# Performance work log

Measured on AMD Instinct MI355X. Metric: run time of the kernel, lower is better.

Reference implementation:

```python
import jax, jax.numpy as jnp
import numpy as np

N = 100_000        # nodes
E = 1_600_000      # edges (avg degree 16)
IN_DIM = 256
OUT_DIM = 32
HEADS = 4
EDGE_DIM = 64
NUM_ETYPES = 8
NEG_SLOPE = 0.2


def setup_inputs() -> dict:
    key = jax.random.key(0)
    ks = jax.random.split(key, 12)
    h = jax.random.normal(ks[0], (N, IN_DIM), dtype=jnp.float32)
    row = jax.random.randint(ks[1], (E,), 0, N, dtype=jnp.int32)
    col = jax.random.randint(ks[2], (E,), 0, N, dtype=jnp.int32)
    etype = jax.random.randint(ks[3], (E,), 0, NUM_ETYPES, dtype=jnp.int32)
    # learned parameters (xavier-ish scale)
    W = jax.random.normal(ks[4], (IN_DIM, OUT_DIM * HEADS), dtype=jnp.float32) * 0.08
    edge_emb = jax.random.normal(ks[5], (NUM_ETYPES, EDGE_DIM), dtype=jnp.float32) * 0.2
    Wr = jax.random.normal(ks[6], (NUM_ETYPES, EDGE_DIM, EDGE_DIM * HEADS), dtype=jnp.float32) * 0.1
    a_l = jax.random.normal(ks[7], (1, HEADS, OUT_DIM), dtype=jnp.float32) * 0.3
    a_r = jax.random.normal(ks[8], (1, HEADS, OUT_DIM), dtype=jnp.float32) * 0.3
    a_e = jax.random.normal(ks[9], (1, HEADS, EDGE_DIM), dtype=jnp.float32) * 0.3
    res_W = jax.random.normal(ks[10], (IN_DIM, OUT_DIM * HEADS), dtype=jnp.float32) * 0.08
    res_b = jnp.zeros((OUT_DIM * HEADS,), dtype=jnp.float32)
    return dict(h=h, W=W, edge_emb=edge_emb, Wr=Wr, a_l=a_l, a_r=a_r, a_e=a_e,
                res_W=res_W, res_b=res_b, row=row, col=col, etype=etype)


def reference(h, W, edge_emb, Wr, a_l, a_r, a_e, res_W, res_b, row, col, etype):
    n = h.shape[0]
    heads, out_dim = a_l.shape[1], a_l.shape[2]
    edge_dim = a_e.shape[2]
    n_etypes = edge_emb.shape[0]

    # node transform: [N, H, D]
    emb = (h @ W).reshape(n, heads, out_dim)
    emb = jnp.where(jnp.isnan(emb), 0.0, emb)

    # typed linear on edge-type embeddings; only num_etypes distinct rows,
    # so compute per type then gather per edge (same math as W_r(edge_emb[etype]))
    e_trans = jnp.einsum('te,tef->tf', edge_emb, Wr).reshape(n_etypes, heads, edge_dim)
    h_e_type = (a_e * e_trans).sum(-1)            # [T, H]

    h_l = (a_l * emb).sum(-1)                     # [N, H]
    h_r = (a_r * emb).sum(-1)                     # [N, H]

    att = h_l[row] + h_r[col] + h_e_type[etype]   # [E, H]
    att = jnp.where(att > 0, att, NEG_SLOPE * att)  # leaky relu

    # edge softmax grouped by destination node (col)
    seg_max = jax.ops.segment_max(att, col, num_segments=n)   # [N, H]
    ex = jnp.exp(att - seg_max[col])
    seg_sum = jax.ops.segment_sum(ex, col, num_segments=n)    # [N, H]
    alpha = ex / seg_sum[col]                                  # [E, H]

    # u_mul_e + sum aggregation; emb permuted to [N, D, H] as in the original
    emb_p = emb.transpose(0, 2, 1)                 # [N, D, H]
    msg = emb_p[row] * alpha[:, None, :]           # [E, D, H]
    agg = jax.ops.segment_sum(msg, col, num_segments=n)  # [N, D, H]
    h_out = agg.reshape(n, out_dim * heads)

    h_out = h_out + h @ res_W + res_b              # residual linear
    return jax.nn.elu(h_out)
```

## Files before the change

kernel.cpp:

```cpp
#include <hip/hip_runtime.h>
#include <math.h>

#define N_NODES   100000
#define N_EDGES   1600000
#define IN_DIM    256
#define OUT_DIM   32
#define HEADS     4
#define C_DIM     128
#define EDGE_DIM  64
#define NUM_ETY   8
#define NEG_SLOPE 0.2f
#define NBLK_SCAN 391
#define M_TILE    128
#define BSTRIDE   40

typedef __attribute__((ext_vector_type(8))) short s8b;
typedef __attribute__((ext_vector_type(4))) float f32x4;
typedef unsigned short ushort_t;

__device__ __forceinline__ short bf16rne(float x) {
    unsigned int u = __float_as_uint(x);
    unsigned int r = (u + 0x7FFFu + ((u >> 16) & 1u)) >> 16;
    return (short)r;
}

__global__ void kz_init(unsigned int* __restrict__ counts) {
    int i = blockIdx.x * blockDim.x + threadIdx.x;
    if (i < N_NODES) counts[i] = 0u;
}

__global__ __launch_bounds__(256) void k_het(
    const float* __restrict__ edge_emb, const float* __restrict__ Wr,
    const float* __restrict__ a_e, float* __restrict__ h_et) {
    __shared__ float ee[EDGE_DIM];
    const int t = threadIdx.x;
    const int ty = blockIdx.x;
    if (t < EDGE_DIM) ee[t] = edge_emb[ty * EDGE_DIM + t];
    __syncthreads();
    const int hh = t >> 6, f = t & 63;
    float acc = 0.f;
#pragma unroll 8
    for (int e = 0; e < EDGE_DIM; ++e)
        acc += ee[e] * Wr[(size_t)(ty * EDGE_DIM + e) * (HEADS * EDGE_DIM) + hh * EDGE_DIM + f];
    acc *= a_e[hh * EDGE_DIM + f];
#pragma unroll
    for (int m = 32; m >= 1; m >>= 1) acc += __shfl_xor(acc, m);
    if (f == 0) h_et[ty * HEADS + hh] = acc;
}

__global__ void kw_prep(const float* __restrict__ W, const float* __restrict__ resW,
                        short* __restrict__ wt) {
    int idx = blockIdx.x * 256 + threadIdx.x;
    int k = idx >> 8, c = idx & 255;
    float v = (c < C_DIM) ? W[k * C_DIM + c] : resW[k * C_DIM + (c - C_DIM)];
    wt[c * IN_DIM + k] = bf16rne(v);
}

__global__ __launch_bounds__(512, 2) void k1_mfma(
    const float* __restrict__ h, const short* __restrict__ wt,
    const float* __restrict__ resb,
    const float* __restrict__ a_l, const float* __restrict__ a_r,
    ushort_t* __restrict__ embh, float* __restrict__ hl, float* __restrict__ hr,
    float* __restrict__ out) {
    __shared__ short hs[M_TILE * IN_DIM];
    __shared__ short bs[2][256 * BSTRIDE];
    const int t  = threadIdx.x;
    const int n0 = blockIdx.x * M_TILE;

#pragma unroll
    for (int i = 0; i < 16; ++i) {
        int f4 = i * 512 + t;
        int row = f4 >> 6, q = f4 & 63;
        int rg = n0 + row;
        float4 v = make_float4(0.f, 0.f, 0.f, 0.f);
        if (rg < N_NODES) v = *(const float4*)&h[(size_t)rg * IN_DIM + q * 4];
        short4 b4;
        b4.x = bf16rne(v.x); b4.y = bf16rne(v.y);
        b4.z = bf16rne(v.z); b4.w = bf16rne(v.w);
        int idx = (row * IN_DIM + q * 4) ^ ((row & 7) << 3);
        *(short4*)&hs[idx] = b4;
    }

    {
        int c = t >> 1, hf = t & 1;
        const s8b* src = (const s8b*)&wt[c * IN_DIM + hf * 16];
        s8b v0 = src[0], v1 = src[1];
        *(s8b*)&bs[0][c * BSTRIDE + hf * 16] = v0;
        *(s8b*)&bs[0][c * BSTRIDE + hf * 16 + 8] = v1;
    }
    __syncthreads();

    const int lane = t & 63, w = t >> 6;
    const int wm = w >> 1;
    const int wn = w & 1;
    const int ln = lane & 15;
    const int kk = lane >> 4;
    const int cstage = t >> 1, hstage = t & 1;

    f32x4 acc[2][8];
#pragma unroll
    for (int mf = 0; mf < 2; ++mf)
#pragma unroll
        for (int nf = 0; nf < 8; ++nf) acc[mf][nf] = (f32x4){0.f, 0.f, 0.f, 0.f};

    int cur = 0;
#pragma unroll
    for (int ks = 0; ks < 8; ++ks) {
        s8b nb0 = {}, nb1 = {};
        if (ks < 7) {
            const s8b* src = (const s8b*)&wt[cstage * IN_DIM + (ks + 1) * 32 + hstage * 16];
            nb0 = src[0];
            nb1 = src[1];
        }

        int r0 = wm * 32 + ln;
        int r1 = wm * 32 + 16 + ln;
        int a0i = (r0 * IN_DIM + ks * 32 + kk * 8) ^ ((r0 & 7) << 3);
        int a1i = (r1 * IN_DIM + ks * 32 + kk * 8) ^ ((r1 & 7) << 3);
        s8b a0 = *(const s8b*)&hs[a0i];
        s8b a1 = *(const s8b*)&hs[a1i];

#pragma unroll
        for (int nf = 0; nf < 8; ++nf) {
            int c = wn * 128 + nf * 16 + ln;
            s8b b = *(const s8b*)&bs[cur][c * BSTRIDE + kk * 8];
            acc[0][nf] = __builtin_amdgcn_mfma_f32_16x16x32_bf16(a0, b, acc[0][nf], 0, 0, 0);
            acc[1][nf] = __builtin_amdgcn_mfma_f32_16x16x32_bf16(a1, b, acc[1][nf], 0, 0, 0);
        }

        if (ks < 7) {
            *(s8b*)&bs[cur ^ 1][cstage * BSTRIDE + hstage * 16] = nb0;
            *(s8b*)&bs[cur ^ 1][cstage * BSTRIDE + hstage * 16 + 8] = nb1;
        }
        __syncthreads();
        cur ^= 1;
    }

    if (wn == 0) {
#pragma unroll
        for (int mf = 0; mf < 2; ++mf)
#pragma unroll
            for (int nf = 0; nf < 8; ++nf) {
                int col = nf * 16 + ln;
#pragma unroll
                for (int r = 0; r < 4; ++r) {
                    int nd = n0 + wm * 32 + mf * 16 + kk * 4 + r;
                    if (nd < N_NODES)
                        embh[(size_t)nd * C_DIM + col] = (ushort_t)bf16rne(acc[mf][nf][r]);
                }
            }
#pragma unroll
        for (int mf = 0; mf < 2; ++mf)
#pragma unroll
            for (int hh = 0; hh < HEADS; ++hh) {
                float al0 = a_l[hh * 32 + ln], al1 = a_l[hh * 32 + 16 + ln];
                float ar0 = a_r[hh * 32 + ln], ar1 = a_r[hh * 32 + 16 + ln];
#pragma unroll
                for (int r = 0; r < 4; ++r) {
                    float pl = al0 * acc[mf][2 * hh][r] + al1 * acc[mf][2 * hh + 1][r];
                    float pr = ar0 * acc[mf][2 * hh][r] + ar1 * acc[mf][2 * hh + 1][r];
#pragma unroll
                    for (int m = 8; m >= 1; m >>= 1) {
                        pl += __shfl_xor(pl, m);
                        pr += __shfl_xor(pr, m);
                    }
                    int nd = n0 + wm * 32 + mf * 16 + kk * 4 + r;
                    if (ln == 0 && nd < N_NODES) {
                        hl[nd * HEADS + hh] = pl;
                        hr[nd * HEADS + hh] = pr;
                    }
                }
            }
    } else {
#pragma unroll
        for (int mf = 0; mf < 2; ++mf)
#pragma unroll
            for (int nf = 0; nf < 8; ++nf) {
                int col = nf * 16 + ln;
                float rb = resb[col];
#pragma unroll
                for (int r = 0; r < 4; ++r) {
                    int nd = n0 + wm * 32 + mf * 16 + kk * 4 + r;
                    if (nd < N_NODES) out[(size_t)nd * C_DIM + col] = acc[mf][nf][r] + rb;
                }
            }
    }
}

__global__ void b1_hist(const int* __restrict__ col, unsigned int* __restrict__ counts) {
    int e = blockIdx.x * blockDim.x + threadIdx.x;
    if (e < N_EDGES) atomicAdd(&counts[col[e]], 1u);
}

__global__ __launch_bounds__(256) void bscan1(const unsigned int* __restrict__ counts,
                                              unsigned int* __restrict__ offs,
                                              unsigned int* __restrict__ bsum) {
    __shared__ unsigned int s[256];
    int t = threadIdx.x;
    int g = blockIdx.x * 256 + t;
    unsigned int v = (g < N_NODES) ? counts[g] : 0u;
    s[t] = v;
    __syncthreads();
    for (int off = 1; off < 256; off <<= 1) {
        unsigned int x = (t >= off) ? s[t - off] : 0u;
        __syncthreads();
        s[t] += x;
        __syncthreads();
    }
    if (g < N_NODES) offs[g] = s[t] - v;
    if (t == 255) bsum[blockIdx.x] = s[255];
}

__global__ __launch_bounds__(512) void bscan2(unsigned int* __restrict__ bsum) {
    __shared__ unsigned int s[512];
    int t = threadIdx.x;
    unsigned int v = (t < NBLK_SCAN) ? bsum[t] : 0u;
    s[t] = v;
    __syncthreads();
    for (int off = 1; off < 512; off <<= 1) {
        unsigned int x = (t >= off) ? s[t - off] : 0u;
        __syncthreads();
        s[t] += x;
        __syncthreads();
    }
    if (t < NBLK_SCAN) bsum[t] = s[t] - v;
}

__global__ void bscan3(unsigned int* __restrict__ offs, const unsigned int* __restrict__ bsum,
                       unsigned int* __restrict__ cursor) {
    int g = blockIdx.x * blockDim.x + threadIdx.x;
    if (g < N_NODES) {
        unsigned int o = offs[g] + bsum[g >> 8];
        offs[g] = o;
        cursor[g] = o;
    }
    if (g == 0) offs[N_NODES] = N_EDGES;
}

__global__ void b4_scatter(const int* __restrict__ row, const int* __restrict__ col,
                           const int* __restrict__ ety,
                           const float* __restrict__ hl, const float* __restrict__ hr,
                           const float* __restrict__ het,
                           unsigned int* __restrict__ cursor,
                           float4* __restrict__ plog, int* __restrict__ prow) {
    int e = blockIdx.x * blockDim.x + threadIdx.x;
    if (e >= N_EDGES) return;
    int r = row[e], c = col[e], ty = ety[e];
    unsigned int pos = atomicAdd(&cursor[c], 1u);
    float4 l  = *(const float4*)&hl[r * 4];
    float4 rr = *(const float4*)&hr[c * 4];
    float4 te = *(const float4*)&het[ty * 4];
    float a0 = l.x + rr.x + te.x;
    float a1 = l.y + rr.y + te.y;
    float a2 = l.z + rr.z + te.z;
    float a3 = l.w + rr.w + te.w;
    a0 = a0 > 0.f ? a0 : NEG_SLOPE * a0;
    a1 = a1 > 0.f ? a1 : NEG_SLOPE * a1;
    a2 = a2 > 0.f ? a2 : NEG_SLOPE * a2;
    a3 = a3 > 0.f ? a3 : NEG_SLOPE * a3;
    plog[pos] = make_float4(a0, a1, a2, a3);
    prow[pos] = r;
}

__device__ __forceinline__ void online_upd(float& m, float& s, float l) {
    float nm = fmaxf(m, l);
    s = s * __expf(m - nm) + __expf(l - nm);
    m = nm;
}

__global__ __launch_bounds__(256) void k_fused(
    const unsigned int* __restrict__ offs, const float4* __restrict__ plog,
    const int* __restrict__ prow, const ushort_t* __restrict__ embh,
    float* __restrict__ out) {
    __shared__ float alds[4][16][4];
    __shared__ int   rlds[4][16];
    const int w    = threadIdx.x >> 6;
    const int lane = threadIdx.x & 63;
    const int c    = blockIdx.x * 4 + w;
    if (c >= N_NODES) return;

    const unsigned int start = offs[c], end = offs[c + 1];

    float m0 = -1e30f, m1 = -1e30f, m2 = -1e30f, m3 = -1e30f;
    float s0 = 0.f, s1 = 0.f, s2 = 0.f, s3 = 0.f;
    for (unsigned int i = start + lane; i < end; i += 64) {
        float4 L = plog[i];
        online_upd(m0, s0, L.x);
        online_upd(m1, s1, L.y);
        online_upd(m2, s2, L.z);
        online_upd(m3, s3, L.w);
    }
#pragma unroll
    for (int off = 32; off >= 1; off >>= 1) {
        float mo, so, nm;
        mo = __shfl_xor(m0, off); so = __shfl_xor(s0, off);
        nm = fmaxf(m0, mo); s0 = s0 * __expf(m0 - nm) + so * __expf(mo - nm); m0 = nm;
        mo = __shfl_xor(m1, off); so = __shfl_xor(s1, off);
        nm = fmaxf(m1, mo); s1 = s1 * __expf(m1 - nm) + so * __expf(mo - nm); m1 = nm;
        mo = __shfl_xor(m2, off); so = __shfl_xor(s2, off);
        nm = fmaxf(m2, mo); s2 = s2 * __expf(m2 - nm) + so * __expf(mo - nm); m2 = nm;
        mo = __shfl_xor(m3, off); so = __shfl_xor(s3, off);
        nm = fmaxf(m3, mo); s3 = s3 * __expf(m3 - nm) + so * __expf(mo - nm); m3 = nm;
    }
    const bool hasE = end > start;
    const float i0 = hasE ? 1.f / s0 : 0.f;
    const float i1 = hasE ? 1.f / s1 : 0.f;
    const float i2 = hasE ? 1.f / s2 : 0.f;
    const float i3 = hasE ? 1.f / s3 : 0.f;

    const int hd = lane >> 4;
    float accA = 0.f, accB = 0.f;

    for (unsigned int base = start; base < end; base += 16) {
        int cnt = (int)min(16u, end - base);
        if (lane < cnt) {
            float4 L = plog[base + lane];
            alds[w][lane][0] = __expf(L.x - m0) * i0;
            alds[w][lane][1] = __expf(L.y - m1) * i1;
            alds[w][lane][2] = __expf(L.z - m2) * i2;
            alds[w][lane][3] = __expf(L.w - m3) * i3;
            rlds[w][lane] = prow[base + lane];
        }
        for (int j = 0; j < cnt; ++j) {
            int r = rlds[w][j];
            float al = alds[w][j][hd];
            unsigned int v = *(const unsigned int*)&embh[(size_t)r * C_DIM + lane * 2];
            float lo = __uint_as_float(v << 16);
            float hi = __uint_as_float(v & 0xffff0000u);
            accA = fmaf(al, lo, accA);
            accB = fmaf(al, hi, accB);
        }
    }

    const int d  = (2 * lane) & 31;
    const int oA = d * 4 + hd;
    const int oB = oA + 4;
    size_t ob = (size_t)c * C_DIM;
    float x0 = out[ob + oA] + accA;
    float x1 = out[ob + oB] + accB;
    out[ob + oA] = x0 > 0.f ? x0 : expm1f(x0);
    out[ob + oB] = x1 > 0.f ? x1 : expm1f(x1);
}

extern "C" void kernel_launch(void* const* d_in, const int* in_sizes, int n_in,
                              void* d_out, int out_size, void* d_ws, size_t ws_size,
                              hipStream_t stream) {
    const float* h        = (const float*)d_in[0];
    const float* W        = (const float*)d_in[1];
    const float* edge_emb = (const float*)d_in[2];
    const float* Wr       = (const float*)d_in[3];
    const float* a_l      = (const float*)d_in[4];
    const float* a_r      = (const float*)d_in[5];
    const float* a_e      = (const float*)d_in[6];
    const float* res_W    = (const float*)d_in[7];
    const float* res_b    = (const float*)d_in[8];
    const int*   row      = (const int*)d_in[9];
    const int*   col      = (const int*)d_in[10];
    const int*   etype    = (const int*)d_in[11];
    float* out = (float*)d_out;

    float* ws = (float*)d_ws;
    float4*       ws_plog  = (float4*)ws;
    float*        p        = ws + (size_t)N_EDGES * 4;
    ushort_t*     ws_embh  = (ushort_t*)p;
    p += (size_t)N_NODES * C_DIM / 2;
    float*        ws_hl    = p;  p += (size_t)N_NODES * HEADS;
    float*        ws_hr    = p;  p += (size_t)N_NODES * HEADS;
    float*        ws_het   = p;  p += 32;
    unsigned int* ws_offs  = (unsigned int*)p;
    unsigned int* ws_cur   = ws_offs + (N_NODES + 1);
    unsigned int* ws_cnt   = ws_cur + N_NODES;
    unsigned int* ws_bsum  = ws_cnt + N_NODES;
    int*          ws_prow  = (int*)(ws_bsum + NBLK_SCAN);
    short*        ws_wt    = (short*)(ws_prow + N_EDGES);

    kz_init<<<(N_NODES + 255) / 256, 256, 0, stream>>>(ws_cnt);

    k_het<<<NUM_ETY, 256, 0, stream>>>(edge_emb, Wr, a_e, ws_het);

    kw_prep<<<256, 256, 0, stream>>>(W, res_W, ws_wt);

    k1_mfma<<<(N_NODES + M_TILE - 1) / M_TILE, 512, 0, stream>>>(
        h, ws_wt, res_b, a_l, a_r, ws_embh, ws_hl, ws_hr, out);

    b1_hist<<<(N_EDGES + 255) / 256, 256, 0, stream>>>(col, ws_cnt);

    bscan1<<<NBLK_SCAN, 256, 0, stream>>>(ws_cnt, ws_offs, ws_bsum);
    bscan2<<<1, 512, 0, stream>>>(ws_bsum);
    bscan3<<<(N_NODES + 255) / 256, 256, 0, stream>>>(ws_offs, ws_bsum, ws_cur);

    b4_scatter<<<(N_EDGES + 255) / 256, 256, 0, stream>>>(
        row, col, etype, ws_hl, ws_hr, ws_het, ws_cur, ws_plog, ws_prow);

    k_fused<<<(N_NODES + 3) / 4, 256, 0, stream>>>(
        ws_offs, ws_plog, ws_prow, ws_embh, out);
}
```

Before: 551.5 us.

## Load GEMM A-operand directly from global memory, dropping LDS staging of h

The node-transform GEMM kernel no longer stages the whole 128x256 bf16 tile of h in shared memory. Each lane now loads its A-fragment float4s straight from global memory every k-step and converts them to bf16 in registers. Removing the 64KB LDS buffer allows raising launch bounds to 4 blocks per CU for more occupancy, and the hand-written bf16 rounding is replaced by the library conversion. The cost is that the two wave columns (wn) load the same h rows from global twice, and global load latency now sits inside the MFMA loop instead of a prologue.

```diff
diff --git a/kernel.cpp b/kernel.cpp
--- a/kernel.cpp
+++ b/kernel.cpp
@@ -1,4 +1,5 @@
 #include <hip/hip_runtime.h>
+#include <hip/hip_bf16.h>
 #include <math.h>
 
 #define N_NODES   100000
@@ -18,10 +19,9 @@
 typedef __attribute__((ext_vector_type(4))) float f32x4;
 typedef unsigned short ushort_t;
 
-__device__ __forceinline__ short bf16rne(float x) {
-    unsigned int u = __float_as_uint(x);
-    unsigned int r = (u + 0x7FFFu + ((u >> 16) & 1u)) >> 16;
-    return (short)r;
+__device__ __forceinline__ short bfc(float x) {
+    __hip_bfloat16 b = __float2bfloat16(x);
+    return *reinterpret_cast<short*>(&b);
 }
 
 __global__ void kz_init(unsigned int* __restrict__ counts) {
@@ -53,40 +53,25 @@
     int idx = blockIdx.x * 256 + threadIdx.x;
     int k = idx >> 8, c = idx & 255;
     float v = (c < C_DIM) ? W[k * C_DIM + c] : resW[k * C_DIM + (c - C_DIM)];
-    wt[c * IN_DIM + k] = bf16rne(v);
-}
-
-__global__ __launch_bounds__(512, 2) void k1_mfma(
+    wt[c * IN_DIM + k] = bfc(v);
+}
+
+__global__ __launch_bounds__(512, 4) void k1_mfma(
     const float* __restrict__ h, const short* __restrict__ wt,
     const float* __restrict__ resb,
     const float* __restrict__ a_l, const float* __restrict__ a_r,
     ushort_t* __restrict__ embh, float* __restrict__ hl, float* __restrict__ hr,
     float* __restrict__ out) {
-    __shared__ short hs[M_TILE * IN_DIM];
     __shared__ short bs[2][256 * BSTRIDE];
     const int t  = threadIdx.x;
     const int n0 = blockIdx.x * M_TILE;
-
-#pragma unroll
-    for (int i = 0; i < 16; ++i) {
-        int f4 = i * 512 + t;
-        int row = f4 >> 6, q = f4 & 63;
-        int rg = n0 + row;
-        float4 v = make_float4(0.f, 0.f, 0.f, 0.f);
-        if (rg < N_NODES) v = *(const float4*)&h[(size_t)rg * IN_DIM + q * 4];
-        short4 b4;
-        b4.x = bf16rne(v.x); b4.y = bf16rne(v.y);
-        b4.z = bf16rne(v.z); b4.w = bf16rne(v.w);
-        int idx = (row * IN_DIM + q * 4) ^ ((row & 7) << 3);
-        *(short4*)&hs[idx] = b4;
-    }
+    const int cstage = t >> 1, hstage = t & 1;
 
     {
-        int c = t >> 1, hf = t & 1;
-        const s8b* src = (const s8b*)&wt[c * IN_DIM + hf * 16];
+        const s8b* src = (const s8b*)&wt[cstage * IN_DIM + hstage * 16];
         s8b v0 = src[0], v1 = src[1];
-        *(s8b*)&bs[0][c * BSTRIDE + hf * 16] = v0;
-        *(s8b*)&bs[0][c * BSTRIDE + hf * 16 + 8] = v1;
+        *(s8b*)&bs[0][cstage * BSTRIDE + hstage * 16] = v0;
+        *(s8b*)&bs[0][cstage * BSTRIDE + hstage * 16 + 8] = v1;
     }
     __syncthreads();
 
@@ -95,7 +80,11 @@
     const int wn = w & 1;
     const int ln = lane & 15;
     const int kk = lane >> 4;
-    const int cstage = t >> 1, hstage = t & 1;
+
+    const int gr0 = min(n0 + wm * 32 + ln, N_NODES - 1);
+    const int gr1 = min(n0 + wm * 32 + 16 + ln, N_NODES - 1);
+    const float* __restrict__ ha0 = &h[(size_t)gr0 * IN_DIM + kk * 8];
+    const float* __restrict__ ha1 = &h[(size_t)gr1 * IN_DIM + kk * 8];
 
     f32x4 acc[2][8];
 #pragma unroll
@@ -113,12 +102,15 @@
             nb1 = src[1];
         }
 
-        int r0 = wm * 32 + ln;
-        int r1 = wm * 32 + 16 + ln;
-        int a0i = (r0 * IN_DIM + ks * 32 + kk * 8) ^ ((r0 & 7) << 3);
-        int a1i = (r1 * IN_DIM + ks * 32 + kk * 8) ^ ((r1 & 7) << 3);
-        s8b a0 = *(const s8b*)&hs[a0i];
-        s8b a1 = *(const s8b*)&hs[a1i];
+        float4 l0 = *(const float4*)&ha0[ks * 32];
+        float4 h0 = *(const float4*)&ha0[ks * 32 + 4];
+        float4 l1 = *(const float4*)&ha1[ks * 32];
+        float4 h1 = *(const float4*)&ha1[ks * 32 + 4];
+        s8b a0, a1;
+        a0[0] = bfc(l0.x); a0[1] = bfc(l0.y); a0[2] = bfc(l0.z); a0[3] = bfc(l0.w);
+        a0[4] = bfc(h0.x); a0[5] = bfc(h0.y); a0[6] = bfc(h0.z); a0[7] = bfc(h0.w);
+        a1[0] = bfc(l1.x); a1[1] = bfc(l1.y); a1[2] = bfc(l1.z); a1[3] = bfc(l1.w);
+        a1[4] = bfc(h1.x); a1[5] = bfc(h1.y); a1[6] = bfc(h1.z); a1[7] = bfc(h1.w);
 
 #pragma unroll
         for (int nf = 0; nf < 8; ++nf) {
@@ -146,7 +138,7 @@
                 for (int r = 0; r < 4; ++r) {
                     int nd = n0 + wm * 32 + mf * 16 + kk * 4 + r;
                     if (nd < N_NODES)
-                        embh[(size_t)nd * C_DIM + col] = (ushort_t)bf16rne(acc[mf][nf][r]);
+                        embh[(size_t)nd * C_DIM + col] = (ushort_t)bfc(acc[mf][nf][r]);
                 }
             }
 #pragma unroll
```

Measured after the change: 530.8 us. -3.8%, faster.
